# Optimization experiments

Measured on AMD Instinct MI355X. Metric: run time of the kernel, lower is better.

Reference implementation:

```python
import jax, jax.numpy as jnp
import numpy as np

N = 8192
D_IN = 128
D_HID = 256  # hard-coded nn.Linear(input_dim, 256) in the module
D_OUT = 64
BN_EPS = 1e-5
LEAKY_SLOPE = 0.01


def setup_inputs() -> dict:
    key = jax.random.key(0)
    k_h, k_a, k_wt, k_wo = jax.random.split(key, 4)
    H = jax.random.normal(k_h, (N, D_IN), dtype=jnp.float32)
    # Fixed adjacency passed to __init__; values in [0,1) so mask=ceil(A*1e-5) is {0,1}
    A = jax.random.uniform(k_a, (N, N), dtype=jnp.float32)
    bn_weight = jnp.ones((D_IN,), jnp.float32)
    bn_bias = jnp.zeros((D_IN,), jnp.float32)
    W_theta = jax.random.normal(k_wt, (D_IN, D_HID), jnp.float32) * np.float32(1.0 / np.sqrt(D_IN))
    b_theta = jnp.zeros((D_HID,), jnp.float32)
    W_out = jax.random.normal(k_wo, (D_IN, D_OUT), jnp.float32) * np.float32(1.0 / np.sqrt(D_IN))
    b_out = jnp.zeros((D_OUT,), jnp.float32)
    return {"H": H, "A": A, "bn_weight": bn_weight, "bn_bias": bn_bias,
            "W_theta": W_theta, "b_theta": b_theta, "W_out": W_out, "b_out": b_out}


def reference(H, A, bn_weight, bn_bias, W_theta, b_theta, W_out, b_out):
    # BatchNorm1d in training mode: biased batch statistics over the node dim
    mean = jnp.mean(H, axis=0)
    var = jnp.mean(jnp.square(H - mean), axis=0)
    Hn = (H - mean) * jax.lax.rsqrt(var + BN_EPS) * bn_weight + bn_bias  # [N, D_IN]

    Hx = Hn @ W_theta + b_theta  # [N, 256]
    mask = jnp.ceil(A * 1e-5)    # constant {0,1} mask from fixed adjacency

    # Dynamic adjacency: clamp(sigmoid(Hx Hx^T), min=0.1) * mask + I
    S = jnp.clip(jax.nn.sigmoid(Hx @ Hx.T), 0.1, None)  # [N, N]
    Ad = S * mask + jnp.eye(N, dtype=H.dtype)

    # D^{-1/2} A D^{-1/2} via broadcast scaling (same math as diag matmuls)
    d = jax.lax.rsqrt(jnp.sum(Ad, axis=1))  # D^{-0.5}, [N]
    A_hat = Ad * d[:, None] * d[None, :]

    out = A_hat @ (Hn @ W_out + b_out)       # [N, D_OUT]
    out = jnp.where(out >= 0, out, LEAKY_SLOPE * out)  # LeakyReLU(0.01)
    return out, A_hat
```

## Files before the change

kernel.cpp:

```cpp
#include <hip/hip_runtime.h>
#include <hip/hip_bf16.h>

#define N 8192
#define DIN 128
#define DHID 256
#define DOUT 64
#define LDP 72
#define VP 136

typedef __attribute__((ext_vector_type(8))) short short8;
typedef __attribute__((ext_vector_type(8))) unsigned short u16x8;
typedef __attribute__((ext_vector_type(4))) float f32x4;
typedef __attribute__((ext_vector_type(4))) unsigned short u16x4;

typedef __attribute__((address_space(1))) const unsigned int GlbU32;
typedef __attribute__((address_space(3))) unsigned int LdsU32;

__device__ inline void gload16(const void* g, void* l) {
  __builtin_amdgcn_global_load_lds((GlbU32*)g, (LdsU32*)l, 16, 0, 0);
}

#define LGKM_BAR()                                            \
  do {                                                        \
    asm volatile("s_waitcnt lgkmcnt(0)" ::: "memory");        \
    __builtin_amdgcn_sched_barrier(0);                        \
    __builtin_amdgcn_s_barrier();                             \
    __builtin_amdgcn_sched_barrier(0);                        \
  } while (0)

__device__ inline unsigned short f2bf(float x) {
  unsigned u = __float_as_uint(x);
  u += 0x7FFF + ((u >> 16) & 1);
  return (unsigned short)(u >> 16);
}
__device__ inline float bf2f(unsigned short u) {
  return __uint_as_float(((unsigned)u) << 16);
}
__device__ inline float sig_clip(float x) {
  float s = 1.0f / (1.0f + __expf(-x));
  return fmaxf(s, 0.1f);
}

__global__ __launch_bounds__(256) void maskpack(const float* __restrict__ A,
                                                unsigned long long* __restrict__ Mb) {
  size_t i = (size_t)blockIdx.x * 256 + threadIdx.x;
  size_t step = (size_t)gridDim.x * 256;
  int l = threadIdx.x & 63;
  for (; i < (size_t)N * N / 4; i += step) {
    f32x4 a = *(const f32x4*)&A[i * 4];
    unsigned long long b0 = __ballot(a[0] > 0.f);
    unsigned long long b1 = __ballot(a[1] > 0.f);
    unsigned long long b2 = __ballot(a[2] > 0.f);
    unsigned long long b3 = __ballot(a[3] > 0.f);
    size_t g = (i - l) >> 6;
    if (l < 4) {
      unsigned long long bb = (l == 0) ? b0 : (l == 1) ? b1 : (l == 2) ? b2 : b3;
      Mb[g * 4 + l] = bb;
    }
  }
}

__global__ void bn_stats(const float* __restrict__ H, const float* __restrict__ bnw,
                         const float* __restrict__ bnb, float* __restrict__ scale,
                         float* __restrict__ shift) {
  int f = blockIdx.x;
  int t = threadIdx.x;
  float s = 0.f, sq = 0.f;
  for (int r = t; r < N; r += 256) {
    float v = H[(size_t)r * DIN + f];
    s += v; sq += v * v;
  }
  __shared__ float ss[256], s2[256];
  ss[t] = s; s2[t] = sq;
  __syncthreads();
  for (int o = 128; o > 0; o >>= 1) {
    if (t < o) { ss[t] += ss[t + o]; s2[t] += s2[t + o]; }
    __syncthreads();
  }
  if (t == 0) {
    float mean = ss[0] * (1.0f / N);
    float var = s2[0] * (1.0f / N) - mean * mean;
    float sc = rsqrtf(var + 1e-5f) * bnw[f];
    scale[f] = sc;
    shift[f] = bnb[f] - mean * sc;
  }
}

__global__ __launch_bounds__(256) void proj(const float* __restrict__ H,
                     const float* __restrict__ scale, const float* __restrict__ shift,
                     const float* __restrict__ Wt, const float* __restrict__ bt,
                     const float* __restrict__ Wo, const float* __restrict__ bo,
                     unsigned short* __restrict__ Hx, unsigned short* __restrict__ M2T) {
  __shared__ float hn[8][DIN];
  int i0 = blockIdx.x * 8;
  int t = threadIdx.x;
  #pragma unroll
  for (int rep = 0; rep < 4; ++rep) {
    int idx = rep * 256 + t;
    int r = idx >> 7, c = idx & 127;
    float h = H[(size_t)(i0 + r) * DIN + c];
    hn[r][c] = fmaf(h, scale[c], shift[c]);
  }
  __syncthreads();
  {
    int c = t;
    float acc[8];
    float b = bt[c];
    #pragma unroll
    for (int r = 0; r < 8; ++r) acc[r] = b;
    for (int k = 0; k < DIN; ++k) {
      float w = Wt[k * DHID + c];
      #pragma unroll
      for (int r = 0; r < 8; ++r) acc[r] = fmaf(hn[r][k], w, acc[r]);
    }
    #pragma unroll
    for (int r = 0; r < 8; ++r) Hx[(size_t)(i0 + r) * DHID + c] = f2bf(acc[r]);
  }
  if (t < DOUT) {
    int c = t;
    float acc[8];
    float b = bo[c];
    #pragma unroll
    for (int r = 0; r < 8; ++r) acc[r] = b;
    for (int k = 0; k < DIN; ++k) {
      float w = Wo[k * DOUT + c];
      #pragma unroll
      for (int r = 0; r < 8; ++r) acc[r] = fmaf(hn[r][k], w, acc[r]);
    }
    u16x8 v;
    #pragma unroll
    for (int r = 0; r < 8; ++r) v[r] = f2bf(acc[r]);
    *(u16x8*)&M2T[(size_t)c * N + i0] = v;
  }
}

template <int BF16V>
__global__ __launch_bounds__(256) void smat(const unsigned short* __restrict__ Hx,
                     const unsigned long long* __restrict__ Mb,
                     float* __restrict__ rowsum,
                     void* __restrict__ Vout) {
  int jt = blockIdx.x, it = blockIdx.y;
  if (BF16V && jt < it) return;
  __shared__ unsigned short lsh[17408];
  __shared__ unsigned mbt32[128][4];
  __shared__ unsigned mbtT[128][4];
  __shared__ float scs[4][128];
  unsigned short* la = lsh;
  unsigned short* lb = lsh + 8192;
  int i0 = it * 128, j0 = jt * 128;
  int t = threadIdx.x;
  int w = t >> 6, l = t & 63;
  int lr = l & 15, lg = l >> 4;
  const bool offdiag = BF16V && (it != jt);

  if (t < 128) {
    const unsigned long long* src = &Mb[(size_t)(i0 + t) * (N / 64) + (j0 >> 8) * 4];
    int sh = (j0 & 128) ? 32 : 0;
    #pragma unroll
    for (int e = 0; e < 4; ++e)
      mbt32[t][e] = (unsigned)(src[e] >> sh);
  }
  if (offdiag && t < 128) {
    const unsigned long long* srcT = &Mb[(size_t)(j0 + t) * (N / 64) + (i0 >> 8) * 4];
    int shT = (i0 & 128) ? 32 : 0;
    #pragma unroll
    for (int e = 0; e < 4; ++e)
      mbtT[t][e] = (unsigned)(srcT[e] >> shT);
  }

  f32x4 acc[2][8];
  f32x4 zero = {0.f, 0.f, 0.f, 0.f};
  #pragma unroll
  for (int m = 0; m < 2; ++m)
    #pragma unroll
    for (int n = 0; n < 8; ++n) acc[m][n] = zero;

  const int srow = l >> 3;
  const int scol = ((l & 7) ^ srow) * 8;
  const int fswz = (lr & 7) * 8;

  for (int c4 = 0; c4 < 4; ++c4) {
    int k0 = c4 * 64;
    __syncthreads();
    #pragma unroll
    for (int rp = 0; rp < 4; ++rp) {
      int chunk = rp * 4 + w;
      int row = chunk * 8 + srow;
      gload16(&Hx[(size_t)(i0 + row) * DHID + k0 + scol], &la[chunk * 512]);
      gload16(&Hx[(size_t)(j0 + row) * DHID + k0 + scol], &lb[chunk * 512]);
    }
    __syncthreads();
    #pragma unroll
    for (int kk = 0; kk < 2; ++kk) {
      int c = (kk * 32 + lg * 8) ^ fswz;
      short8 af[2], bf[8];
      #pragma unroll
      for (int m = 0; m < 2; ++m)
        af[m] = *(const short8*)&la[(w * 32 + m * 16 + lr) * 64 + c];
      #pragma unroll
      for (int n = 0; n < 8; ++n)
        bf[n] = *(const short8*)&lb[(n * 16 + lr) * 64 + c];
      #pragma unroll
      for (int m = 0; m < 2; ++m)
        #pragma unroll
        for (int n = 0; n < 8; ++n)
          acc[m][n] = __builtin_amdgcn_mfma_f32_16x16x32_bf16(af[m], bf[n], acc[m][n], 0, 0, 0);
    }
  }

  if (BF16V) __syncthreads();

  #pragma unroll
  for (int m = 0; m < 2; ++m) {
    #pragma unroll
    for (int r = 0; r < 4; ++r) {
      int rl = w * 32 + m * 16 + lg * 4 + r;
      int gi = i0 + rl;
      unsigned mw = mbt32[rl][lr & 3];
      float part = 0.f;
      #pragma unroll
      for (int n = 0; n < 8; ++n) {
        int gj = j0 + n * 16 + lr;
        float ms = ((mw >> (n * 4 + (lr >> 2))) & 1u) ? 1.f : 0.f;
        float v = sig_clip(acc[m][n][r]) * ms + (gi == gj ? 1.f : 0.f);
        part += v;
        if (BF16V)
          lsh[rl * VP + n * 16 + lr] = f2bf(v);
        else
          ((float*)Vout)[(size_t)gi * N + gj] = v;
      }
      part += __shfl_xor(part, 1);
      part += __shfl_xor(part, 2);
      part += __shfl_xor(part, 4);
      part += __shfl_xor(part, 8);
      if (lr == 0) atomicAdd(&rowsum[gi], part);
    }
  }

  if (BF16V) {
    __syncthreads();
    #pragma unroll
    for (int pass = 0; pass < 8; ++pass) {
      int row = pass * 16 + (t >> 4);
      int cc = (t & 15) * 8;
      u16x8 vv = *(const u16x8*)&lsh[row * VP + cc];
      *(u16x8*)&((unsigned short*)Vout)[(size_t)(i0 + row) * N + j0 + cc] = vv;
    }
  }

  if (offdiag) {
    __syncthreads();
    float p[8];
    #pragma unroll
    for (int n = 0; n < 8; ++n) p[n] = 0.f;
    #pragma unroll
    for (int m = 0; m < 2; ++m) {
      #pragma unroll
      for (int r = 0; r < 4; ++r) {
        int rl = w * 32 + m * 16 + lg * 4 + r;
        int bitp = w * 8 + m * 4 + lg;
        #pragma unroll
        for (int n = 0; n < 8; ++n) {
          int c = n * 16 + lr;
          float ms = ((mbtT[c][r] >> bitp) & 1u) ? 1.f : 0.f;
          float v = sig_clip(acc[m][n][r]) * ms;
          p[n] += v;
          lsh[c * VP + rl] = f2bf(v);
        }
      }
    }
    #pragma unroll
    for (int n = 0; n < 8; ++n) {
      p[n] += __shfl_xor(p[n], 16);
      p[n] += __shfl_xor(p[n], 32);
    }
    if (lg == 0) {
      #pragma unroll
      for (int n = 0; n < 8; ++n) scs[w][n * 16 + lr] = p[n];
    }
    __syncthreads();
    if (t < 128) {
      float cs = scs[0][t] + scs[1][t] + scs[2][t] + scs[3][t];
      atomicAdd(&rowsum[j0 + t], cs);
    }
    #pragma unroll
    for (int pass = 0; pass < 8; ++pass) {
      int row = pass * 16 + (t >> 4);
      int cc = (t & 15) * 8;
      u16x8 vv = *(const u16x8*)&lsh[row * VP + cc];
      *(u16x8*)&((unsigned short*)Vout)[(size_t)(j0 + row) * N + i0 + cc] = vv;
    }
  }
}

__global__ void dfin(float* rs) {
  int i = blockIdx.x * 256 + threadIdx.x;
  if (i < N) rs[i] = rsqrtf(rs[i]);
}

template <int BF16V>
__global__ __launch_bounds__(256) void outmm(const void* __restrict__ Vin,
                      const float* __restrict__ dd,
                      const unsigned short* __restrict__ M2T,
                      float* __restrict__ Ahat, float* __restrict__ out) {
  __shared__ unsigned short la[2][128 * LDP];
  int kc = blockIdx.x;
  int it = blockIdx.y;
  int i0 = it * 128;
  int jbase = kc * 512;
  int t = threadIdx.x;
  int w = t >> 6, l = t & 63;
  int lr = l & 15, lg = l >> 4;

  f32x4 acc[2][4];
  f32x4 zero = {0.f, 0.f, 0.f, 0.f};
  #pragma unroll
  for (int m = 0; m < 2; ++m)
    #pragma unroll
    for (int n = 0; n < 4; ++n) acc[m][n] = zero;

  if (BF16V) {
    const unsigned short* V = (const unsigned short*)Vin;
    const int row8 = t >> 3;
    const int cc8 = (t & 7) * 8;

    float di[4];
    #pragma unroll
    for (int rep = 0; rep < 4; ++rep) di[rep] = dd[i0 + rep * 32 + row8];

    u16x8 u[2][4];
    #pragma unroll
    for (int rep = 0; rep < 4; ++rep)
      u[0][rep] = *(const u16x8*)&V[(size_t)(i0 + rep * 32 + row8) * N + jbase + cc8];

    #pragma unroll
    for (int s = 0; s < 8; ++s) {
      const int cur = s & 1;
      const int j0 = jbase + s * 64;
      if (s < 7) {
        #pragma unroll
        for (int rep = 0; rep < 4; ++rep)
          u[cur ^ 1][rep] = *(const u16x8*)&V[(size_t)(i0 + rep * 32 + row8) * N + j0 + 64 + cc8];
      }
      short8 bfr[2][4];
      #pragma unroll
      for (int kk = 0; kk < 2; ++kk)
        #pragma unroll
        for (int n = 0; n < 4; ++n)
          bfr[kk][n] = *(const short8*)&M2T[(size_t)(n * 16 + lr) * N + j0 + kk * 32 + lg * 8];
      f32x4 dj0 = *(const f32x4*)&dd[j0 + cc8];
      f32x4 dj1 = *(const f32x4*)&dd[j0 + cc8 + 4];
      #pragma unroll
      for (int rep = 0; rep < 4; ++rep) {
        int row = rep * 32 + row8;
        size_t idx = (size_t)(i0 + row) * N + j0 + cc8;
        f32x4 s0, s1;
        s0[0] = bf2f(u[cur][rep][0]) * di[rep] * dj0[0];
        s0[1] = bf2f(u[cur][rep][1]) * di[rep] * dj0[1];
        s0[2] = bf2f(u[cur][rep][2]) * di[rep] * dj0[2];
        s0[3] = bf2f(u[cur][rep][3]) * di[rep] * dj0[3];
        s1[0] = bf2f(u[cur][rep][4]) * di[rep] * dj1[0];
        s1[1] = bf2f(u[cur][rep][5]) * di[rep] * dj1[1];
        s1[2] = bf2f(u[cur][rep][6]) * di[rep] * dj1[2];
        s1[3] = bf2f(u[cur][rep][7]) * di[rep] * dj1[3];
        *(f32x4*)&Ahat[idx] = s0;
        *(f32x4*)&Ahat[idx + 4] = s1;
        u16x8 b;
        b[0] = f2bf(s0[0]); b[1] = f2bf(s0[1]); b[2] = f2bf(s0[2]); b[3] = f2bf(s0[3]);
        b[4] = f2bf(s1[0]); b[5] = f2bf(s1[1]); b[6] = f2bf(s1[2]); b[7] = f2bf(s1[3]);
        *(u16x8*)&la[cur][row * LDP + cc8] = b;
      }
      LGKM_BAR();
      #pragma unroll
      for (int kk = 0; kk < 2; ++kk) {
        short8 af[2];
        #pragma unroll
        for (int m = 0; m < 2; ++m)
          af[m] = *(const short8*)&la[cur][(w * 32 + m * 16 + lr) * LDP + kk * 32 + lg * 8];
        #pragma unroll
        for (int m = 0; m < 2; ++m)
          #pragma unroll
          for (int n = 0; n < 4; ++n)
            acc[m][n] = __builtin_amdgcn_mfma_f32_16x16x32_bf16(af[m], bfr[kk][n], acc[m][n], 0, 0, 0);
      }
    }
  } else {
    for (int s = 0; s < 8; ++s) {
      int j0 = jbase + s * 64;
      __syncthreads();
      #pragma unroll
      for (int rep = 0; rep < 8; ++rep) {
        int row = rep * 16 + (t >> 4);
        int cc = (t & 15) * 4;
        size_t idx = (size_t)(i0 + row) * N + j0 + cc;
        f32x4 v = *(const f32x4*)&((const float*)Vin)[idx];
        float dii = dd[i0 + row];
        f32x4 dj = *(const f32x4*)&dd[j0 + cc];
        f32x4 sv;
        sv[0] = v[0] * dii * dj[0]; sv[1] = v[1] * dii * dj[1];
        sv[2] = v[2] * dii * dj[2]; sv[3] = v[3] * dii * dj[3];
        *(f32x4*)&Ahat[idx] = sv;
        u16x4 b;
        b[0] = f2bf(sv[0]); b[1] = f2bf(sv[1]); b[2] = f2bf(sv[2]); b[3] = f2bf(sv[3]);
        *(u16x4*)&la[0][row * LDP + cc] = b;
      }
      __syncthreads();
      #pragma unroll
      for (int kk = 0; kk < 2; ++kk) {
        short8 af[2], bfr[4];
        #pragma unroll
        for (int m = 0; m < 2; ++m)
          af[m] = *(const short8*)&la[0][(w * 32 + m * 16 + lr) * LDP + kk * 32 + lg * 8];
        #pragma unroll
        for (int n = 0; n < 4; ++n)
          bfr[n] = *(const short8*)&M2T[(size_t)(n * 16 + lr) * N + j0 + kk * 32 + lg * 8];
        #pragma unroll
        for (int m = 0; m < 2; ++m)
          #pragma unroll
          for (int n = 0; n < 4; ++n)
            acc[m][n] = __builtin_amdgcn_mfma_f32_16x16x32_bf16(af[m], bfr[n], acc[m][n], 0, 0, 0);
      }
    }
  }

  #pragma unroll
  for (int m = 0; m < 2; ++m)
    #pragma unroll
    for (int n = 0; n < 4; ++n)
      #pragma unroll
      for (int r = 0; r < 4; ++r) {
        int gi = i0 + w * 32 + m * 16 + lg * 4 + r;
        int gc = n * 16 + lr;
        atomicAdd(&out[(size_t)gi * DOUT + gc], acc[m][n][r]);
      }
}

__global__ void leaky(float* out) {
  int i = blockIdx.x * 256 + threadIdx.x;
  if (i < N * DOUT) {
    float x = out[i];
    out[i] = x >= 0.f ? x : 0.01f * x;
  }
}

extern "C" void kernel_launch(void* const* d_in, const int* in_sizes, int n_in,
                              void* d_out, int out_size, void* d_ws, size_t ws_size,
                              hipStream_t stream) {
  const float* H   = (const float*)d_in[0];
  const float* A   = (const float*)d_in[1];
  const float* bnw = (const float*)d_in[2];
  const float* bnb = (const float*)d_in[3];
  const float* Wt  = (const float*)d_in[4];
  const float* bt  = (const float*)d_in[5];
  const float* Wo  = (const float*)d_in[6];
  const float* bo  = (const float*)d_in[7];
  float* out = (float*)d_out;
  float* Ahat = out + (size_t)N * DOUT;

  char* ws = (char*)d_ws;
  float* scale  = (float*)(ws + 0);
  float* shift  = (float*)(ws + 512);
  float* rowsum = (float*)(ws + 4096);
  unsigned short* M2T = (unsigned short*)(ws + 65536);
  unsigned short* Hx  = (unsigned short*)(ws + 2097152);
  unsigned long long* Mb = (unsigned long long*)(ws + (size_t)(6u << 20));
  unsigned short* Vbf = (unsigned short*)(ws + (size_t)(14u << 20));

  const size_t need_bf16 = ((size_t)14 << 20) + (size_t)N * N * 2;
  const bool big = ws_size >= need_bf16;

  hipMemsetAsync(rowsum, 0, N * sizeof(float), stream);
  hipMemsetAsync(out, 0, (size_t)N * DOUT * sizeof(float), stream);

  maskpack<<<4096, 256, 0, stream>>>(A, Mb);
  bn_stats<<<DIN, 256, 0, stream>>>(H, bnw, bnb, scale, shift);
  proj<<<N / 8, 256, 0, stream>>>(H, scale, shift, Wt, bt, Wo, bo, Hx, M2T);
  if (big) {
    smat<1><<<dim3(64, 64), 256, 0, stream>>>(Hx, Mb, rowsum, (void*)Vbf);
    dfin<<<N / 256, 256, 0, stream>>>(rowsum);
    outmm<1><<<dim3(16, 64), 256, 0, stream>>>((const void*)Vbf, rowsum, M2T, Ahat, out);
  } else {
    smat<0><<<dim3(64, 64), 256, 0, stream>>>(Hx, Mb, rowsum, (void*)Ahat);
    dfin<<<N / 256, 256, 0, stream>>>(rowsum);
    outmm<0><<<dim3(16, 64), 256, 0, stream>>>((const void*)Ahat, rowsum, M2T, Ahat, out);
  }
  leaky<<<(N * DOUT + 255) / 256, 256, 0, stream>>>(out);
}
```

Measured before the change: 318.8 us.

## Recompute similarity matrix in final pass instead of storing bf16 intermediate

The first pass now only computes row sums of the masked sigmoid matrix (upper-triangle tiles, symmetric accumulation) without writing any N×N intermediate. A new fused final kernel recomputes Hx·Hxᵀ per tile, applies mask, diagonal and degree scaling, writes A_hat in fp32 and immediately multiplies the bf16 tile by M2T. This removes the 128MB bf16 write and read of V in exchange for doing the N×N×256 GEMM twice. The final kernel's grid drops to 512 blocks, each walking 8 column tiles serially.

```diff
diff --git a/kernel.cpp b/kernel.cpp
--- a/kernel.cpp
+++ b/kernel.cpp
@@ -5,13 +5,12 @@
 #define DIN 128
 #define DHID 256
 #define DOUT 64
-#define LDP 72
 #define VP 136
 
 typedef __attribute__((ext_vector_type(8))) short short8;
 typedef __attribute__((ext_vector_type(8))) unsigned short u16x8;
 typedef __attribute__((ext_vector_type(4))) float f32x4;
-typedef __attribute__((ext_vector_type(4))) unsigned short u16x4;
+typedef __attribute__((ext_vector_type(2))) unsigned long long u64x2;
 
 typedef __attribute__((address_space(1))) const unsigned int GlbU32;
 typedef __attribute__((address_space(3))) unsigned int LdsU32;
@@ -32,9 +31,6 @@
   unsigned u = __float_as_uint(x);
   u += 0x7FFF + ((u >> 16) & 1);
   return (unsigned short)(u >> 16);
-}
-__device__ inline float bf2f(unsigned short u) {
-  return __uint_as_float(((unsigned)u) << 16);
 }
 __device__ inline float sig_clip(float x) {
   float s = 1.0f / (1.0f + __expf(-x));
@@ -134,14 +130,12 @@
   }
 }
 
-template <int BF16V>
-__global__ __launch_bounds__(256) void smat(const unsigned short* __restrict__ Hx,
+__global__ __launch_bounds__(256) void rsum(const unsigned short* __restrict__ Hx,
                      const unsigned long long* __restrict__ Mb,
-                     float* __restrict__ rowsum,
-                     void* __restrict__ Vout) {
+                     float* __restrict__ rowsum) {
   int jt = blockIdx.x, it = blockIdx.y;
-  if (BF16V && jt < it) return;
-  __shared__ unsigned short lsh[17408];
+  if (jt < it) return;
+  __shared__ unsigned short lsh[16384];
   __shared__ unsigned mbt32[128][4];
   __shared__ unsigned mbtT[128][4];
   __shared__ float scs[4][128];
@@ -151,7 +145,7 @@
   int t = threadIdx.x;
   int w = t >> 6, l = t & 63;
   int lr = l & 15, lg = l >> 4;
-  const bool offdiag = BF16V && (it != jt);
+  const bool offdiag = (it != jt);
 
   if (t < 128) {
     const unsigned long long* src = &Mb[(size_t)(i0 + t) * (N / 64) + (j0 >> 8) * 4];
@@ -208,8 +202,6 @@
     }
   }
 
-  if (BF16V) __syncthreads();
-
   #pragma unroll
   for (int m = 0; m < 2; ++m) {
     #pragma unroll
@@ -222,12 +214,7 @@
       for (int n = 0; n < 8; ++n) {
         int gj = j0 + n * 16 + lr;
         float ms = ((mw >> (n * 4 + (lr >> 2))) & 1u) ? 1.f : 0.f;
-        float v = sig_clip(acc[m][n][r]) * ms + (gi == gj ? 1.f : 0.f);
-        part += v;
-        if (BF16V)
-          lsh[rl * VP + n * 16 + lr] = f2bf(v);
-        else
-          ((float*)Vout)[(size_t)gi * N + gj] = v;
+        part += sig_clip(acc[m][n][r]) * ms + (gi == gj ? 1.f : 0.f);
       }
       part += __shfl_xor(part, 1);
       part += __shfl_xor(part, 2);
@@ -237,19 +224,7 @@
     }
   }
 
-  if (BF16V) {
-    __syncthreads();
-    #pragma unroll
-    for (int pass = 0; pass < 8; ++pass) {
-      int row = pass * 16 + (t >> 4);
-      int cc = (t & 15) * 8;
-      u16x8 vv = *(const u16x8*)&lsh[row * VP + cc];
-      *(u16x8*)&((unsigned short*)Vout)[(size_t)(i0 + row) * N + j0 + cc] = vv;
-    }
-  }
-
   if (offdiag) {
-    __syncthreads();
     float p[8];
     #pragma unroll
     for (int n = 0; n < 8; ++n) p[n] = 0.f;
@@ -257,15 +232,12 @@
     for (int m = 0; m < 2; ++m) {
       #pragma unroll
       for (int r = 0; r < 4; ++r) {
-        int rl = w * 32 + m * 16 + lg * 4 + r;
         int bitp = w * 8 + m * 4 + lg;
         #pragma unroll
         for (int n = 0; n < 8; ++n) {
           int c = n * 16 + lr;
           float ms = ((mbtT[c][r] >> bitp) & 1u) ? 1.f : 0.f;
-          float v = sig_clip(acc[m][n][r]) * ms;
-          p[n] += v;
-          lsh[c * VP + rl] = f2bf(v);
+          p[n] += sig_clip(acc[m][n][r]) * ms;
         }
       }
     }
@@ -283,13 +255,6 @@
       float cs = scs[0][t] + scs[1][t] + scs[2][t] + scs[3][t];
       atomicAdd(&rowsum[j0 + t], cs);
     }
-    #pragma unroll
-    for (int pass = 0; pass < 8; ++pass) {
-      int row = pass * 16 + (t >> 4);
-      int cc = (t & 15) * 8;
-      u16x8 vv = *(const u16x8*)&lsh[row * VP + cc];
-      *(u16x8*)&((unsigned short*)Vout)[(size_t)(j0 + row) * N + i0 + cc] = vv;
-    }
   }
 }
 
@@ -298,128 +263,153 @@
   if (i < N) rs[i] = rsqrtf(rs[i]);
 }
 
-template <int BF16V>
-__global__ __launch_bounds__(256) void outmm(const void* __restrict__ Vin,
-                      const float* __restrict__ dd,
-                      const unsigned short* __restrict__ M2T,
-                      float* __restrict__ Ahat, float* __restrict__ out) {
-  __shared__ unsigned short la[2][128 * LDP];
-  int kc = blockIdx.x;
-  int it = blockIdx.y;
-  int i0 = it * 128;
-  int jbase = kc * 512;
-  int t = threadIdx.x;
-  int w = t >> 6, l = t & 63;
-  int lr = l & 15, lg = l >> 4;
-
-  f32x4 acc[2][4];
+__global__ __launch_bounds__(256) void finmm(const unsigned short* __restrict__ Hx,
+                     const unsigned long long* __restrict__ Mb,
+                     const float* __restrict__ dd,
+                     const unsigned short* __restrict__ M2T,
+                     float* __restrict__ Ahat, float* __restrict__ out) {
+  __shared__ unsigned short lsh[25600];
+  __shared__ unsigned mbt32[128][4];
+  unsigned short* lb = lsh;
+  unsigned short* lVb = lsh + 8192;
+  const int blk = blockIdx.x;
+  const int jq = blk & 7;
+  const int it = blk >> 3;
+  const int i0 = it * 128;
+  const int t = threadIdx.x;
+  const int w = t >> 6, l = t & 63;
+  const int lr = l & 15, lg = l >> 4;
+  const int srow = l >> 3;
+  const int scol = ((l & 7) ^ srow) * 8;
+  const int fswz = (lr & 7) * 8;
+
+  short8 af[2][8];
+  #pragma unroll
+  for (int h = 0; h < 2; ++h) {
+    __syncthreads();
+    #pragma unroll
+    for (int itr = 0; itr < 8; ++itr) {
+      int idx = itr * 4 + w;
+      int c4 = idx >> 3, rg = idx & 7;
+      int row = h * 64 + rg * 8 + srow;
+      gload16(&Hx[(size_t)(i0 + row) * DHID + c4 * 64 + scol], &lsh[idx * 512]);
+    }
+    __syncthreads();
+    if ((w >> 1) == h) {
+      #pragma unroll
+      for (int c4 = 0; c4 < 4; ++c4)
+        #pragma unroll
+        for (int kk = 0; kk < 2; ++kk)
+          #pragma unroll
+          for (int m = 0; m < 2; ++m)
+            af[m][c4 * 2 + kk] = *(const short8*)&lsh[c4 * 4096 +
+                ((w & 1) * 32 + m * 16 + lr) * 64 + ((kk * 32 + lg * 8) ^ fswz)];
+    }
+  }
+  __syncthreads();
+
+  float di[2][4];
+  #pragma unroll
+  for (int m = 0; m < 2; ++m)
+    #pragma unroll
+    for (int r = 0; r < 4; ++r)
+      di[m][r] = dd[i0 + w * 32 + m * 16 + lg * 4 + r];
+
+  {
+    int j0 = jq * 8 * 128;
+    int mrow = t >> 1, ep = (t & 1) * 2;
+    u64x2 mv = *(const u64x2*)&Mb[(size_t)(i0 + mrow) * (N / 64) + (j0 >> 8) * 4 + ep];
+    int sh = (j0 & 128) ? 32 : 0;
+    mbt32[mrow][ep] = (unsigned)(mv[0] >> sh);
+    mbt32[mrow][ep + 1] = (unsigned)(mv[1] >> sh);
+  }
+
+  f32x4 acc2[2][4];
   f32x4 zero = {0.f, 0.f, 0.f, 0.f};
   #pragma unroll
   for (int m = 0; m < 2; ++m)
     #pragma unroll
-    for (int n = 0; n < 4; ++n) acc[m][n] = zero;
-
-  if (BF16V) {
-    const unsigned short* V = (const unsigned short*)Vin;
-    const int row8 = t >> 3;
-    const int cc8 = (t & 7) * 8;
-
-    float di[4];
-    #pragma unroll
-    for (int rep = 0; rep < 4; ++rep) di[rep] = dd[i0 + rep * 32 + row8];
-
-    u16x8 u[2][4];
-    #pragma unroll
-    for (int rep = 0; rep < 4; ++rep)
-      u[0][rep] = *(const u16x8*)&V[(size_t)(i0 + rep * 32 + row8) * N + jbase + cc8];
-
-    #pragma unroll
-    for (int s = 0; s < 8; ++s) {
-      const int cur = s & 1;
-      const int j0 = jbase + s * 64;
-      if (s < 7) {
-        #pragma unroll
-        for (int rep = 0; rep < 4; ++rep)
-          u[cur ^ 1][rep] = *(const u16x8*)&V[(size_t)(i0 + rep * 32 + row8) * N + j0 + 64 + cc8];
-      }
-      short8 bfr[2][4];
-      #pragma unroll
-      for (int kk = 0; kk < 2; ++kk)
-        #pragma unroll
-        for (int n = 0; n < 4; ++n)
-          bfr[kk][n] = *(const short8*)&M2T[(size_t)(n * 16 + lr) * N + j0 + kk * 32 + lg * 8];
-      f32x4 dj0 = *(const f32x4*)&dd[j0 + cc8];
-      f32x4 dj1 = *(const f32x4*)&dd[j0 + cc8 + 4];
-      #pragma unroll
-      for (int rep = 0; rep < 4; ++rep) {
-        int row = rep * 32 + row8;
-        size_t idx = (size_t)(i0 + row) * N + j0 + cc8;
-        f32x4 s0, s1;
-        s0[0] = bf2f(u[cur][rep][0]) * di[rep] * dj0[0];
-        s0[1] = bf2f(u[cur][rep][1]) * di[rep] * dj0[1];
-        s0[2] = bf2f(u[cur][rep][2]) * di[rep] * dj0[2];
-        s0[3] = bf2f(u[cur][rep][3]) * di[rep] * dj0[3];
-        s1[0] = bf2f(u[cur][rep][4]) * di[rep] * dj1[0];
-        s1[1] = bf2f(u[cur][rep][5]) * di[rep] * dj1[1];
-        s1[2] = bf2f(u[cur][rep][6]) * di[rep] * dj1[2];
-        s1[3] = bf2f(u[cur][rep][7]) * di[rep] * dj1[3];
-        *(f32x4*)&Ahat[idx] = s0;
-        *(f32x4*)&Ahat[idx + 4] = s1;
-        u16x8 b;
-        b[0] = f2bf(s0[0]); b[1] = f2bf(s0[1]); b[2] = f2bf(s0[2]); b[3] = f2bf(s0[3]);
-        b[4] = f2bf(s1[0]); b[5] = f2bf(s1[1]); b[6] = f2bf(s1[2]); b[7] = f2bf(s1[3]);
-        *(u16x8*)&la[cur][row * LDP + cc8] = b;
-      }
-      LGKM_BAR();
+    for (int n = 0; n < 4; ++n) acc2[m][n] = zero;
+
+  for (int jtl = 0; jtl < 8; ++jtl) {
+    const int j0 = (jq * 8 + jtl) * 128;
+    f32x4 acc[2][8];
+    #pragma unroll
+    for (int m = 0; m < 2; ++m)
+      #pragma unroll
+      for (int n = 0; n < 8; ++n) acc[m][n] = zero;
+
+    #pragma unroll
+    for (int c4 = 0; c4 < 4; ++c4) {
+      __syncthreads();
+      #pragma unroll
+      for (int itr = 0; itr < 4; ++itr) {
+        int rg = itr * 4 + w;
+        int row = rg * 8 + srow;
+        gload16(&Hx[(size_t)(j0 + row) * DHID + c4 * 64 + scol], &lb[rg * 512]);
+      }
+      __syncthreads();
       #pragma unroll
       for (int kk = 0; kk < 2; ++kk) {
-        short8 af[2];
-        #pragma unroll
-        for (int m = 0; m < 2; ++m)
-          af[m] = *(const short8*)&la[cur][(w * 32 + m * 16 + lr) * LDP + kk * 32 + lg * 8];
+        int c = (kk * 32 + lg * 8) ^ fswz;
+        short8 bf[8];
+        #pragma unroll
+        for (int n = 0; n < 8; ++n)
+          bf[n] = *(const short8*)&lb[(n * 16 + lr) * 64 + c];
         #pragma unroll
         for (int m = 0; m < 2; ++m)
           #pragma unroll
-          for (int n = 0; n < 4; ++n)
-            acc[m][n] = __builtin_amdgcn_mfma_f32_16x16x32_bf16(af[m], bfr[kk][n], acc[m][n], 0, 0, 0);
-      }
-    }
-  } else {
-    for (int s = 0; s < 8; ++s) {
-      int j0 = jbase + s * 64;
-      __syncthreads();
-      #pragma unroll
-      for (int rep = 0; rep < 8; ++rep) {
-        int row = rep * 16 + (t >> 4);
-        int cc = (t & 15) * 4;
-        size_t idx = (size_t)(i0 + row) * N + j0 + cc;
-        f32x4 v = *(const f32x4*)&((const float*)Vin)[idx];
-        float dii = dd[i0 + row];
-        f32x4 dj = *(const f32x4*)&dd[j0 + cc];
-        f32x4 sv;
-        sv[0] = v[0] * dii * dj[0]; sv[1] = v[1] * dii * dj[1];
-        sv[2] = v[2] * dii * dj[2]; sv[3] = v[3] * dii * dj[3];
-        *(f32x4*)&Ahat[idx] = sv;
-        u16x4 b;
-        b[0] = f2bf(sv[0]); b[1] = f2bf(sv[1]); b[2] = f2bf(sv[2]); b[3] = f2bf(sv[3]);
-        *(u16x4*)&la[0][row * LDP + cc] = b;
-      }
-      __syncthreads();
-      #pragma unroll
-      for (int kk = 0; kk < 2; ++kk) {
-        short8 af[2], bfr[4];
-        #pragma unroll
-        for (int m = 0; m < 2; ++m)
-          af[m] = *(const short8*)&la[0][(w * 32 + m * 16 + lr) * LDP + kk * 32 + lg * 8];
+          for (int n = 0; n < 8; ++n)
+            acc[m][n] = __builtin_amdgcn_mfma_f32_16x16x32_bf16(af[m][c4 * 2 + kk], bf[n], acc[m][n], 0, 0, 0);
+      }
+    }
+
+    float dj[8];
+    #pragma unroll
+    for (int n = 0; n < 8; ++n) dj[n] = dd[j0 + n * 16 + lr];
+    #pragma unroll
+    for (int m = 0; m < 2; ++m) {
+      #pragma unroll
+      for (int r = 0; r < 4; ++r) {
+        int rl = w * 32 + m * 16 + lg * 4 + r;
+        int gi = i0 + rl;
+        unsigned mw = mbt32[rl][lr & 3];
+        #pragma unroll
+        for (int n = 0; n < 8; ++n) {
+          int gj = j0 + n * 16 + lr;
+          float ms = ((mw >> (n * 4 + (lr >> 2))) & 1u) ? 1.f : 0.f;
+          float v = sig_clip(acc[m][n][r]) * ms + (gi == gj ? 1.f : 0.f);
+          float a = v * di[m][r] * dj[n];
+          Ahat[(size_t)gi * N + gj] = a;
+          lVb[rl * VP + n * 16 + lr] = f2bf(a);
+        }
+      }
+    }
+    LGKM_BAR();
+
+    #pragma unroll
+    for (int kk2 = 0; kk2 < 4; ++kk2) {
+      short8 af2[2], bfr[4];
+      #pragma unroll
+      for (int m = 0; m < 2; ++m)
+        af2[m] = *(const short8*)&lVb[(w * 32 + m * 16 + lr) * VP + kk2 * 32 + lg * 8];
+      #pragma unroll
+      for (int n = 0; n < 4; ++n)
+        bfr[n] = *(const short8*)&M2T[(size_t)(n * 16 + lr) * N + j0 + kk2 * 32 + lg * 8];
+      #pragma unroll
+      for (int m = 0; m < 2; ++m)
         #pragma unroll
         for (int n = 0; n < 4; ++n)
-          bfr[n] = *(const short8*)&M2T[(size_t)(n * 16 + lr) * N + j0 + kk * 32 + lg * 8];
-        #pragma unroll
-        for (int m = 0; m < 2; ++m)
-          #pragma unroll
-          for (int n = 0; n < 4; ++n)
-            acc[m][n] = __builtin_amdgcn_mfma_f32_16x16x32_bf16(af[m], bfr[n], acc[m][n], 0, 0, 0);
-      }
+          acc2[m][n] = __builtin_amdgcn_mfma_f32_16x16x32_bf16(af2[m], bfr[n], acc2[m][n], 0, 0, 0);
+    }
+
+    if (jtl < 7) {
+      int nj0 = (jq * 8 + jtl + 1) * 128;
+      int mrow = t >> 1, ep = (t & 1) * 2;
+      u64x2 mv = *(const u64x2*)&Mb[(size_t)(i0 + mrow) * (N / 64) + (nj0 >> 8) * 4 + ep];
+      int sh = (nj0 & 128) ? 32 : 0;
+      mbt32[mrow][ep] = (unsigned)(mv[0] >> sh);
+      mbt32[mrow][ep + 1] = (unsigned)(mv[1] >> sh);
     }
   }
 
@@ -431,7 +421,7 @@
       for (int r = 0; r < 4; ++r) {
         int gi = i0 + w * 32 + m * 16 + lg * 4 + r;
         int gc = n * 16 + lr;
-        atomicAdd(&out[(size_t)gi * DOUT + gc], acc[m][n][r]);
+        atomicAdd(&out[(size_t)gi * DOUT + gc], acc2[m][n][r]);
       }
 }
 
@@ -464,10 +454,6 @@
   unsigned short* M2T = (unsigned short*)(ws + 65536);
   unsigned short* Hx  = (unsigned short*)(ws + 2097152);
   unsigned long long* Mb = (unsigned long long*)(ws + (size_t)(6u << 20));
-  unsigned short* Vbf = (unsigned short*)(ws + (size_t)(14u << 20));
-
-  const size_t need_bf16 = ((size_t)14 << 20) + (size_t)N * N * 2;
-  const bool big = ws_size >= need_bf16;
 
   hipMemsetAsync(rowsum, 0, N * sizeof(float), stream);
   hipMemsetAsync(out, 0, (size_t)N * DOUT * sizeof(float), stream);
@@ -475,14 +461,8 @@
   maskpack<<<4096, 256, 0, stream>>>(A, Mb);
   bn_stats<<<DIN, 256, 0, stream>>>(H, bnw, bnb, scale, shift);
   proj<<<N / 8, 256, 0, stream>>>(H, scale, shift, Wt, bt, Wo, bo, Hx, M2T);
-  if (big) {
-    smat<1><<<dim3(64, 64), 256, 0, stream>>>(Hx, Mb, rowsum, (void*)Vbf);
-    dfin<<<N / 256, 256, 0, stream>>>(rowsum);
-    outmm<1><<<dim3(16, 64), 256, 0, stream>>>((const void*)Vbf, rowsum, M2T, Ahat, out);
-  } else {
-    smat<0><<<dim3(64, 64), 256, 0, stream>>>(Hx, Mb, rowsum, (void*)Ahat);
-    dfin<<<N / 256, 256, 0, stream>>>(rowsum);
-    outmm<0><<<dim3(16, 64), 256, 0, stream>>>((const void*)Ahat, rowsum, M2T, Ahat, out);
-  }
+  rsum<<<dim3(64, 64), 256, 0, stream>>>(Hx, Mb, rowsum);
+  dfin<<<N / 256, 256, 0, stream>>>(rowsum);
+  finmm<<<512, 256, 0, stream>>>(Hx, Mb, rowsum, M2T, Ahat, out);
   leaky<<<(N * DOUT + 255) / 256, 256, 0, stream>>>(out);
 }
```

Result: slower. 373.4 us (+17.1%).
